# Kernel tuning notes

Measured on AMD Instinct MI355X. Metric: run time of the kernel, lower is better.

The kernel has to match this reference:

```python
import jax, jax.numpy as jnp
import numpy as np
from math import sqrt


def setup_inputs() -> dict:
    key = jax.random.key(0)
    kq, kk, kv = jax.random.split(key, 3)
    B, L, H, E = 4, 2048, 8, 64
    S, D = L, E
    return {
        "queries": jax.random.normal(kq, (B, L, H, E), dtype=jnp.float32),
        "keys": jax.random.normal(kk, (B, S, H, E), dtype=jnp.float32),
        "values": jax.random.normal(kv, (B, S, H, D), dtype=jnp.float32),
    }


def reference(queries, keys, values):
    # FullAttention with mask_flag=True (TriangularCausalMask), dropout p=0,
    # output_attention=False. scale = 1/sqrt(E).
    B, L, H, E = queries.shape
    S = keys.shape[1]
    scale = 1.0 / sqrt(E)
    # scores: [B, H, L, S]
    scores = jnp.einsum("blhe,bshe->bhls", queries, keys)
    # causal mask: positions s > l are masked (upper triangle above diagonal)
    causal = jnp.tril(jnp.ones((L, S), dtype=bool))  # True = keep
    neg_inf = jnp.finfo(scores.dtype).min
    scores = jnp.where(causal, scores, neg_inf)
    A = jax.nn.softmax(scale * scores, axis=-1)  # [B,H,L,S]
    # context: [B, L, H, D]
    V = jnp.einsum("bhls,bshd->blhd", A, values)
    return V
```

## Files before the change

kernel.cpp:

```cpp
#include <hip/hip_runtime.h>
#include <math.h>

#define BD 4
#define LD 2048
#define HD 8
#define ED 64
#define TQ 128
#define TK 64
#define RS (HD * ED)

typedef __attribute__((ext_vector_type(8))) _Float16 f16x8;
typedef __attribute__((ext_vector_type(4))) _Float16 f16x4;
typedef __attribute__((ext_vector_type(4))) float f32x4;
typedef __attribute__((ext_vector_type(4))) unsigned int u32x4;
typedef __attribute__((ext_vector_type(2))) unsigned int u32x2;
typedef unsigned int u32;
typedef unsigned long long u64;

__device__ inline u32 pkh(float a, float b) {
    return __builtin_bit_cast(u32, __builtin_amdgcn_cvt_pkrtz(a, b));
}
__device__ inline u64 pkh4(float a, float b, float c, float d) {
    return (u64)pkh(a, b) | ((u64)pkh(c, d) << 32);
}
__device__ inline int swz(int row, int bcol) {
    return row * 128 + ((((bcol >> 4) ^ row) & 7) << 4) + (bcol & 15);
}

__global__ __launch_bounds__(256, 2)
void fa_mfma_k16(const float* __restrict__ Q, const float* __restrict__ K,
                 const float* __restrict__ V, float* __restrict__ O) {
    __shared__ __align__(16) char smem[32768];

    const int t    = threadIdx.x;
    const int lane = t & 63;
    const int w    = t >> 6;
    const int m16  = lane & 15;
    const int quad = lane >> 4;

    const int b = blockIdx.x >> 3;
    const int h = blockIdx.x & 7;
    const int y   = (int)blockIdx.y;
    const int qtp = (y < 8) ? (15 - y) : (y - 8);
    const int q0  = qtp * TQ;
    const int kmax = 2 * qtp + 1;

    const int ks  = t >> 2;
    const int ke0 = (t & 3) << 2;
    const int vs0 = (t & 15) << 2;
    const int vd0 = (t >> 4) << 2;

    const float* Kbase = K + ((size_t)((b * LD + ks) * HD + h)) * ED + ke0;
    const float* Vbase = V + ((size_t)((b * LD + vs0) * HD + h)) * ED + vd0;

    const float qscale = 0.125f * 1.44269504088896340736f;
    f16x8 qf[2][2];
    #pragma unroll
    for (int sub = 0; sub < 2; ++sub) {
        const float* qrow =
            Q + ((size_t)((b * LD + q0 + (w << 5) + (sub << 4) + m16) * HD + h)) * ED;
        #pragma unroll
        for (int hf = 0; hf < 2; ++hf) {
            const float4 x = *(const float4*)(qrow + hf * 32 + quad * 8);
            const float4 y4 = *(const float4*)(qrow + hf * 32 + quad * 8 + 4);
            u32x4 p;
            p[0] = pkh(x.x * qscale, x.y * qscale);
            p[1] = pkh(x.z * qscale, x.w * qscale);
            p[2] = pkh(y4.x * qscale, y4.y * qscale);
            p[3] = pkh(y4.z * qscale, y4.w * qscale);
            qf[sub][hf] = __builtin_bit_cast(f16x8, p);
        }
    }

    f32x4 oacc[2][4];
    float l_i[2] = {0.0f, 0.0f};
    #pragma unroll
    for (int sub = 0; sub < 2; ++sub)
        #pragma unroll
        for (int nt = 0; nt < 4; ++nt) oacc[sub][nt] = (f32x4){0.f, 0.f, 0.f, 0.f};

    float4 kx[4], vx[4];
    {
        #pragma unroll
        for (int j = 0; j < 4; ++j) kx[j] = *(const float4*)(Kbase + 16 * j);
        #pragma unroll
        for (int r = 0; r < 4; ++r) vx[r] = *(const float4*)(Vbase + r * RS);
        char* wK = smem;
        char* wV = smem + 16384;
        #pragma unroll
        for (int j = 0; j < 4; ++j)
            *(u64*)(wK + swz(ks, 2 * (ke0 + 16 * j))) = pkh4(kx[j].x, kx[j].y, kx[j].z, kx[j].w);
        *(u64*)(wV + swz(vd0 + 0, 2 * vs0)) = pkh4(vx[0].x, vx[1].x, vx[2].x, vx[3].x);
        *(u64*)(wV + swz(vd0 + 1, 2 * vs0)) = pkh4(vx[0].y, vx[1].y, vx[2].y, vx[3].y);
        *(u64*)(wV + swz(vd0 + 2, 2 * vs0)) = pkh4(vx[0].z, vx[1].z, vx[2].z, vx[3].z);
        *(u64*)(wV + swz(vd0 + 3, 2 * vs0)) = pkh4(vx[0].w, vx[1].w, vx[2].w, vx[3].w);
    }
    __syncthreads();

    for (int kt = 0; kt <= kmax; ++kt) {
        char* rK = smem + ((kt & 1) << 13);
        char* rV = smem + 16384 + ((kt & 1) << 13);
        const bool pre = kt < kmax;

        if (pre) {
            const float* kp = Kbase + (size_t)(kt + 1) * (TK * RS);
            const float* vp = Vbase + (size_t)(kt + 1) * (TK * RS);
            #pragma unroll
            for (int j = 0; j < 4; ++j) kx[j] = *(const float4*)(kp + 16 * j);
            #pragma unroll
            for (int r = 0; r < 4; ++r) vx[r] = *(const float4*)(vp + r * RS);
        }

        const int offq = (2 * qtp - kt) * 64;
        if (offq + (w << 5) + 31 >= 0) {
            f32x4 sacc[2][4];
            #pragma unroll
            for (int kc = 0; kc < 4; ++kc) {
                const f16x8 kf0 = *(const f16x8*)(rK + swz(kc * 16 + m16, quad * 16));
                const f16x8 kf1 = *(const f16x8*)(rK + swz(kc * 16 + m16, 64 + quad * 16));
                #pragma unroll
                for (int sub = 0; sub < 2; ++sub) {
                    f32x4 z = {0.f, 0.f, 0.f, 0.f};
                    z = __builtin_amdgcn_mfma_f32_16x16x32_f16(kf0, qf[sub][0], z, 0, 0, 0);
                    z = __builtin_amdgcn_mfma_f32_16x16x32_f16(kf1, qf[sub][1], z, 0, 0, 0);
                    sacc[sub][kc] = z;
                }
            }

            if (offq < 64) {
                #pragma unroll
                for (int sub = 0; sub < 2; ++sub) {
                    const int ql = (w << 5) + (sub << 4) + m16 + offq;
                    #pragma unroll
                    for (int kc = 0; kc < 4; ++kc)
                        #pragma unroll
                        for (int i = 0; i < 4; ++i)
                            if (kc * 16 + quad * 4 + i > ql) sacc[sub][kc][i] = -INFINITY;
                }
            }

            f16x4 pf[2][4];
            #pragma unroll
            for (int sub = 0; sub < 2; ++sub) {
                #pragma unroll
                for (int kc = 0; kc < 4; ++kc) {
                    float p0 = __builtin_amdgcn_exp2f(sacc[sub][kc][0]);
                    float p1 = __builtin_amdgcn_exp2f(sacc[sub][kc][1]);
                    float p2 = __builtin_amdgcn_exp2f(sacc[sub][kc][2]);
                    float p3 = __builtin_amdgcn_exp2f(sacc[sub][kc][3]);
                    l_i[sub] += (p0 + p1) + (p2 + p3);
                    u32x2 pp;
                    pp[0] = pkh(p0, p1);
                    pp[1] = pkh(p2, p3);
                    pf[sub][kc] = __builtin_bit_cast(f16x4, pp);
                }
            }

            #pragma unroll
            for (int kc = 0; kc < 4; ++kc) {
                #pragma unroll
                for (int dt = 0; dt < 4; ++dt) {
                    const f16x4 vf = *(const f16x4*)
                        (rV + swz(dt * 16 + m16, 2 * (kc * 16 + quad * 4)));
                    oacc[0][dt] = __builtin_amdgcn_mfma_f32_16x16x16f16(vf, pf[0][kc], oacc[0][dt], 0, 0, 0);
                    oacc[1][dt] = __builtin_amdgcn_mfma_f32_16x16x16f16(vf, pf[1][kc], oacc[1][dt], 0, 0, 0);
                }
            }
        }

        if (pre) {
            char* wK = smem + ((kt & 1) ? 0 : 8192);
            char* wV = smem + 16384 + ((kt & 1) ? 0 : 8192);
            #pragma unroll
            for (int j = 0; j < 4; ++j)
                *(u64*)(wK + swz(ks, 2 * (ke0 + 16 * j))) = pkh4(kx[j].x, kx[j].y, kx[j].z, kx[j].w);
            *(u64*)(wV + swz(vd0 + 0, 2 * vs0)) = pkh4(vx[0].x, vx[1].x, vx[2].x, vx[3].x);
            *(u64*)(wV + swz(vd0 + 1, 2 * vs0)) = pkh4(vx[0].y, vx[1].y, vx[2].y, vx[3].y);
            *(u64*)(wV + swz(vd0 + 2, 2 * vs0)) = pkh4(vx[0].z, vx[1].z, vx[2].z, vx[3].z);
            *(u64*)(wV + swz(vd0 + 3, 2 * vs0)) = pkh4(vx[0].w, vx[1].w, vx[2].w, vx[3].w);
        }
        __syncthreads();
    }

    #pragma unroll
    for (int sub = 0; sub < 2; ++sub) {
        float l = l_i[sub];
        l += __shfl_xor(l, 16);
        l += __shfl_xor(l, 32);
        const float inv = 1.0f / l;
        float* orow =
            O + ((size_t)((b * LD + q0 + (w << 5) + (sub << 4) + m16) * HD + h)) * ED;
        #pragma unroll
        for (int dt = 0; dt < 4; ++dt) {
            float4 o;
            o.x = oacc[sub][dt][0] * inv;
            o.y = oacc[sub][dt][1] * inv;
            o.z = oacc[sub][dt][2] * inv;
            o.w = oacc[sub][dt][3] * inv;
            *(float4*)(orow + dt * 16 + quad * 4) = o;
        }
    }
}

extern "C" void kernel_launch(void* const* d_in, const int* in_sizes, int n_in,
                              void* d_out, int out_size, void* d_ws, size_t ws_size,
                              hipStream_t stream) {
    const float* Q = (const float*)d_in[0];
    const float* K = (const float*)d_in[1];
    const float* V = (const float*)d_in[2];
    float* O = (float*)d_out;
    dim3 grid(BD * HD, LD / TQ);
    fa_mfma_k16<<<grid, 256, 0, stream>>>(Q, K, V, O);
}
```

Baseline: 122.4 us.

## Split KV range across two blocks and combine bf16 partials in second kernel

Splits each query tile's causal key range into two halves processed by separate blocks (grid z=2). Each half writes unnormalized bf16 partial outputs and row sums to workspace, and a combine kernel sums them and normalizes. Occupancy hint is raised to 4 blocks per CU. The aim is to double the number of blocks and balance the causal workload. The cost is an extra kernel launch, the workspace traffic, and bf16 rounding of the partials. The split is safe without a max rescale only because the kernel already skips the running max and relies on the fixed scaled score range.

```diff
diff --git a/kernel.cpp b/kernel.cpp
--- a/kernel.cpp
+++ b/kernel.cpp
@@ -23,13 +23,23 @@
 __device__ inline u64 pkh4(float a, float b, float c, float d) {
     return (u64)pkh(a, b) | ((u64)pkh(c, d) << 32);
 }
+__device__ inline u32 f2bf(float f) {
+    u32 u = __builtin_bit_cast(u32, f);
+    u += 0x7fffu + ((u >> 16) & 1u);
+    return u >> 16;
+}
+__device__ inline float b2f(unsigned short s) {
+    return __builtin_bit_cast(float, (u32)s << 16);
+}
 __device__ inline int swz(int row, int bcol) {
     return row * 128 + ((((bcol >> 4) ^ row) & 7) << 4) + (bcol & 15);
 }
 
-__global__ __launch_bounds__(256, 2)
-void fa_mfma_k16(const float* __restrict__ Q, const float* __restrict__ K,
-                 const float* __restrict__ V, float* __restrict__ O) {
+template<int NSPLIT>
+__global__ __launch_bounds__(256, 4)
+void fa_fwd(const float* __restrict__ Q, const float* __restrict__ K,
+            const float* __restrict__ V, float* __restrict__ O,
+            unsigned short* __restrict__ Op, float* __restrict__ lp) {
     __shared__ __align__(16) char smem[32768];
 
     const int t    = threadIdx.x;
@@ -43,7 +53,10 @@
     const int y   = (int)blockIdx.y;
     const int qtp = (y < 8) ? (15 - y) : (y - 8);
     const int q0  = qtp * TQ;
-    const int kmax = 2 * qtp + 1;
+    const int split  = (int)blockIdx.z;
+    const int cnt    = (2 * qtp + 2) / NSPLIT;
+    const int kt0    = split * cnt;
+    const int kt_end = kt0 + cnt - 1;
 
     const int ks  = t >> 2;
     const int ke0 = (t & 3) << 2;
@@ -77,16 +90,18 @@
     #pragma unroll
     for (int sub = 0; sub < 2; ++sub)
         #pragma unroll
-        for (int nt = 0; nt < 4; ++nt) oacc[sub][nt] = (f32x4){0.f, 0.f, 0.f, 0.f};
+        for (int dt = 0; dt < 4; ++dt) oacc[sub][dt] = (f32x4){0.f, 0.f, 0.f, 0.f};
 
     float4 kx[4], vx[4];
     {
-        #pragma unroll
-        for (int j = 0; j < 4; ++j) kx[j] = *(const float4*)(Kbase + 16 * j);
-        #pragma unroll
-        for (int r = 0; r < 4; ++r) vx[r] = *(const float4*)(Vbase + r * RS);
-        char* wK = smem;
-        char* wV = smem + 16384;
+        const float* kp = Kbase + (size_t)kt0 * (TK * RS);
+        const float* vp = Vbase + (size_t)kt0 * (TK * RS);
+        #pragma unroll
+        for (int j = 0; j < 4; ++j) kx[j] = *(const float4*)(kp + 16 * j);
+        #pragma unroll
+        for (int r = 0; r < 4; ++r) vx[r] = *(const float4*)(vp + r * RS);
+        char* wK = smem + ((kt0 & 1) << 13);
+        char* wV = smem + 16384 + ((kt0 & 1) << 13);
         #pragma unroll
         for (int j = 0; j < 4; ++j)
             *(u64*)(wK + swz(ks, 2 * (ke0 + 16 * j))) = pkh4(kx[j].x, kx[j].y, kx[j].z, kx[j].w);
@@ -97,10 +112,10 @@
     }
     __syncthreads();
 
-    for (int kt = 0; kt <= kmax; ++kt) {
+    for (int kt = kt0; kt <= kt_end; ++kt) {
         char* rK = smem + ((kt & 1) << 13);
         char* rV = smem + 16384 + ((kt & 1) << 13);
-        const bool pre = kt < kmax;
+        const bool pre = kt < kt_end;
 
         if (pre) {
             const float* kp = Kbase + (size_t)(kt + 1) * (TK * RS);
@@ -144,10 +159,10 @@
             for (int sub = 0; sub < 2; ++sub) {
                 #pragma unroll
                 for (int kc = 0; kc < 4; ++kc) {
-                    float p0 = __builtin_amdgcn_exp2f(sacc[sub][kc][0]);
-                    float p1 = __builtin_amdgcn_exp2f(sacc[sub][kc][1]);
-                    float p2 = __builtin_amdgcn_exp2f(sacc[sub][kc][2]);
-                    float p3 = __builtin_amdgcn_exp2f(sacc[sub][kc][3]);
+                    const float p0 = __builtin_amdgcn_exp2f(sacc[sub][kc][0]);
+                    const float p1 = __builtin_amdgcn_exp2f(sacc[sub][kc][1]);
+                    const float p2 = __builtin_amdgcn_exp2f(sacc[sub][kc][2]);
+                    const float p3 = __builtin_amdgcn_exp2f(sacc[sub][kc][3]);
                     l_i[sub] += (p0 + p1) + (p2 + p3);
                     u32x2 pp;
                     pp[0] = pkh(p0, p1);
@@ -169,8 +184,8 @@
         }
 
         if (pre) {
-            char* wK = smem + ((kt & 1) ? 0 : 8192);
-            char* wV = smem + 16384 + ((kt & 1) ? 0 : 8192);
+            char* wK = smem + (((kt & 1) ^ 1) << 13);
+            char* wV = smem + 16384 + (((kt & 1) ^ 1) << 13);
             #pragma unroll
             for (int j = 0; j < 4; ++j)
                 *(u64*)(wK + swz(ks, 2 * (ke0 + 16 * j))) = pkh4(kx[j].x, kx[j].y, kx[j].z, kx[j].w);
@@ -187,19 +202,54 @@
         float l = l_i[sub];
         l += __shfl_xor(l, 16);
         l += __shfl_xor(l, 32);
-        const float inv = 1.0f / l;
-        float* orow =
-            O + ((size_t)((b * LD + q0 + (w << 5) + (sub << 4) + m16) * HD + h)) * ED;
-        #pragma unroll
-        for (int dt = 0; dt < 4; ++dt) {
-            float4 o;
-            o.x = oacc[sub][dt][0] * inv;
-            o.y = oacc[sub][dt][1] * inv;
-            o.z = oacc[sub][dt][2] * inv;
-            o.w = oacc[sub][dt][3] * inv;
-            *(float4*)(orow + dt * 16 + quad * 4) = o;
-        }
-    }
+        const int q = q0 + (w << 5) + (sub << 4) + m16;
+        if (NSPLIT == 1) {
+            const float inv = 1.0f / l;
+            float* orow = O + ((size_t)((b * LD + q) * HD + h)) * ED;
+            #pragma unroll
+            for (int dt = 0; dt < 4; ++dt) {
+                float4 o;
+                o.x = oacc[sub][dt][0] * inv;
+                o.y = oacc[sub][dt][1] * inv;
+                o.z = oacc[sub][dt][2] * inv;
+                o.w = oacc[sub][dt][3] * inv;
+                *(float4*)(orow + dt * 16 + quad * 4) = o;
+            }
+        } else {
+            unsigned short* prow = Op + (size_t)split * (BD * LD * HD * ED)
+                                      + ((size_t)((b * LD + q) * HD + h)) * ED;
+            #pragma unroll
+            for (int dt = 0; dt < 4; ++dt) {
+                const u64 pk = (u64)(f2bf(oacc[sub][dt][0]) | (f2bf(oacc[sub][dt][1]) << 16))
+                             | ((u64)(f2bf(oacc[sub][dt][2]) | (f2bf(oacc[sub][dt][3]) << 16)) << 32);
+                *(u64*)(prow + dt * 16 + quad * 4) = pk;
+            }
+            if (quad == 0)
+                lp[(size_t)split * (BD * HD * LD) + (b * HD + h) * LD + q] = l;
+        }
+    }
+}
+
+__global__ __launch_bounds__(256)
+void fa_combine(const unsigned short* __restrict__ Op,
+                const float* __restrict__ lp, float* __restrict__ O) {
+    const int tid = blockIdx.x * 256 + threadIdx.x;
+    const int rid = tid >> 4;
+    const int h   = rid & 7;
+    const int bq  = rid >> 3;
+    const int b   = bq >> 11;
+    const int q   = bq & 2047;
+    const int lidx = (b * HD + h) * LD + q;
+    const float inv = 1.0f / (lp[lidx] + lp[BD * HD * LD + lidx]);
+    const size_t i = (size_t)tid * 4;
+    const ushort4 a = *(const ushort4*)(Op + i);
+    const ushort4 c = *(const ushort4*)(Op + (size_t)(BD * LD * HD * ED) + i);
+    float4 o;
+    o.x = (b2f(a.x) + b2f(c.x)) * inv;
+    o.y = (b2f(a.y) + b2f(c.y)) * inv;
+    o.z = (b2f(a.z) + b2f(c.z)) * inv;
+    o.w = (b2f(a.w) + b2f(c.w)) * inv;
+    *(float4*)(O + i) = o;
 }
 
 extern "C" void kernel_launch(void* const* d_in, const int* in_sizes, int n_in,
@@ -209,6 +259,17 @@
     const float* K = (const float*)d_in[1];
     const float* V = (const float*)d_in[2];
     float* O = (float*)d_out;
-    dim3 grid(BD * HD, LD / TQ);
-    fa_mfma_k16<<<grid, 256, 0, stream>>>(Q, K, V, O);
-}
+    const size_t PSZ = (size_t)BD * LD * HD * ED;
+    const size_t need = 2 * PSZ * sizeof(unsigned short)
+                      + 2 * (size_t)BD * HD * LD * sizeof(float);
+    if (ws_size >= need) {
+        unsigned short* Op = (unsigned short*)d_ws;
+        float* lp = (float*)((char*)d_ws + 2 * PSZ * sizeof(unsigned short));
+        dim3 g1(BD * HD, 16, 2);
+        fa_fwd<2><<<g1, 256, 0, stream>>>(Q, K, V, nullptr, Op, lp);
+        fa_combine<<<(int)(PSZ / 4 / 256), 256, 0, stream>>>(Op, lp, O);
+    } else {
+        dim3 g1(BD * HD, 16, 1);
+        fa_fwd<1><<<g1, 256, 0, stream>>>(Q, K, V, O, nullptr, nullptr);
+    }
+}
```

After: 193.7 us. +58.3%, slower.

## Pre-convert K/V to swizzled fp16 tiles and stream them via direct-to-LDS loads

Applied to the files above, without the earlier changes.

Adds a prep kernel that converts K and V to fp16 once per tile, writing them into the swizzled (and, for V, transposed) shared-memory image in a workspace. The main kernel then fills shared memory with global_load_lds DMA copies instead of loading fp32, converting and storing through registers. It also halves the query tile to 64 rows with 128-thread blocks, which doubles the block count. This is meant to remove the repeated fp32 K/V reads and the per-block conversion cost. In exchange it adds a second launch and a workspace round trip, and it relies on the workspace being large enough.

```diff
diff --git a/kernel.cpp b/kernel.cpp
--- a/kernel.cpp
+++ b/kernel.cpp
@@ -5,9 +5,10 @@
 #define LD 2048
 #define HD 8
 #define ED 64
-#define TQ 128
+#define TQ 64
 #define TK 64
 #define RS (HD * ED)
+#define NTILE (BD * HD * 32)
 
 typedef __attribute__((ext_vector_type(8))) _Float16 f16x8;
 typedef __attribute__((ext_vector_type(4))) _Float16 f16x4;
@@ -20,16 +21,62 @@
 __device__ inline u32 pkh(float a, float b) {
     return __builtin_bit_cast(u32, __builtin_amdgcn_cvt_pkrtz(a, b));
 }
-__device__ inline u64 pkh4(float a, float b, float c, float d) {
-    return (u64)pkh(a, b) | ((u64)pkh(c, d) << 32);
-}
 __device__ inline int swz(int row, int bcol) {
     return row * 128 + ((((bcol >> 4) ^ row) & 7) << 4) + (bcol & 15);
 }
-
-__global__ __launch_bounds__(256, 2)
-void fa_mfma_k16(const float* __restrict__ Q, const float* __restrict__ K,
-                 const float* __restrict__ V, float* __restrict__ O) {
+__device__ inline void dma16(const void* g, void* l) {
+    __builtin_amdgcn_global_load_lds(
+        (const __attribute__((address_space(1))) u32*)g,
+        (__attribute__((address_space(3))) u32*)l, 16, 0, 0);
+}
+
+__global__ __launch_bounds__(256, 4)
+void fa_prep(const float* __restrict__ K, const float* __restrict__ V,
+             unsigned short* __restrict__ Kh, unsigned short* __restrict__ Vh) {
+    __shared__ __align__(16) char vimg[8192];
+    const int bid = blockIdx.x;
+    const int kt  = bid & 31;
+    const int bh  = bid >> 5;
+    const int b   = bh >> 3;
+    const int h   = bh & 7;
+    const int t   = threadIdx.x;
+    const int s   = t >> 2;
+    const int e0  = (t & 3) << 4;
+
+    const float* krow = K + ((size_t)((b * LD + kt * TK + s) * HD + h)) * ED + e0;
+    const float* vrow = V + ((size_t)((b * LD + kt * TK + s) * HD + h)) * ED + e0;
+
+    char* kimg = (char*)(Kh + (size_t)bid * 4096);
+    #pragma unroll
+    for (int j = 0; j < 2; ++j) {
+        const float4 x = *(const float4*)(krow + 8 * j);
+        const float4 y = *(const float4*)(krow + 8 * j + 4);
+        u32x4 p;
+        p[0] = pkh(x.x, x.y); p[1] = pkh(x.z, x.w);
+        p[2] = pkh(y.x, y.y); p[3] = pkh(y.z, y.w);
+        *(u32x4*)(kimg + swz(s, 2 * e0 + 16 * j)) = p;
+    }
+
+    float va[16];
+    #pragma unroll
+    for (int j = 0; j < 4; ++j) {
+        const float4 x = *(const float4*)(vrow + 4 * j);
+        va[4 * j + 0] = x.x; va[4 * j + 1] = x.y;
+        va[4 * j + 2] = x.z; va[4 * j + 3] = x.w;
+    }
+    #pragma unroll
+    for (int c = 0; c < 16; ++c)
+        *(_Float16*)(vimg + swz(e0 + c, 2 * s)) = (_Float16)va[c];
+    __syncthreads();
+
+    char* vout = (char*)(Vh + (size_t)bid * 4096);
+    *(u32x4*)(vout + t * 32)      = *(const u32x4*)(vimg + t * 32);
+    *(u32x4*)(vout + t * 32 + 16) = *(const u32x4*)(vimg + t * 32 + 16);
+}
+
+__global__ __launch_bounds__(128, 2)
+void fa_main(const float* __restrict__ Q, const unsigned short* __restrict__ Kh,
+             const unsigned short* __restrict__ Vh, float* __restrict__ O) {
     __shared__ __align__(16) char smem[32768];
 
     const int t    = threadIdx.x;
@@ -40,18 +87,12 @@
 
     const int b = blockIdx.x >> 3;
     const int h = blockIdx.x & 7;
-    const int y   = (int)blockIdx.y;
-    const int qtp = (y < 8) ? (15 - y) : (y - 8);
-    const int q0  = qtp * TQ;
-    const int kmax = 2 * qtp + 1;
-
-    const int ks  = t >> 2;
-    const int ke0 = (t & 3) << 2;
-    const int vs0 = (t & 15) << 2;
-    const int vd0 = (t >> 4) << 2;
-
-    const float* Kbase = K + ((size_t)((b * LD + ks) * HD + h)) * ED + ke0;
-    const float* Vbase = V + ((size_t)((b * LD + vs0) * HD + h)) * ED + vd0;
+    const int y  = (int)blockIdx.y;
+    const int qt = (y < 16) ? (31 - y) : (y - 16);
+    const int q0 = qt * TQ;
+
+    const char* Kt = (const char*)(Kh + ((size_t)(b * 8 + h) * 32) * 4096);
+    const char* Vt = (const char*)(Vh + ((size_t)(b * 8 + h) * 32) * 4096);
 
     const float qscale = 0.125f * 1.44269504088896340736f;
     f16x8 qf[2][2];
@@ -77,108 +118,85 @@
     #pragma unroll
     for (int sub = 0; sub < 2; ++sub)
         #pragma unroll
-        for (int nt = 0; nt < 4; ++nt) oacc[sub][nt] = (f32x4){0.f, 0.f, 0.f, 0.f};
-
-    float4 kx[4], vx[4];
-    {
-        #pragma unroll
-        for (int j = 0; j < 4; ++j) kx[j] = *(const float4*)(Kbase + 16 * j);
-        #pragma unroll
-        for (int r = 0; r < 4; ++r) vx[r] = *(const float4*)(Vbase + r * RS);
-        char* wK = smem;
-        char* wV = smem + 16384;
-        #pragma unroll
-        for (int j = 0; j < 4; ++j)
-            *(u64*)(wK + swz(ks, 2 * (ke0 + 16 * j))) = pkh4(kx[j].x, kx[j].y, kx[j].z, kx[j].w);
-        *(u64*)(wV + swz(vd0 + 0, 2 * vs0)) = pkh4(vx[0].x, vx[1].x, vx[2].x, vx[3].x);
-        *(u64*)(wV + swz(vd0 + 1, 2 * vs0)) = pkh4(vx[0].y, vx[1].y, vx[2].y, vx[3].y);
-        *(u64*)(wV + swz(vd0 + 2, 2 * vs0)) = pkh4(vx[0].z, vx[1].z, vx[2].z, vx[3].z);
-        *(u64*)(wV + swz(vd0 + 3, 2 * vs0)) = pkh4(vx[0].w, vx[1].w, vx[2].w, vx[3].w);
-    }
+        for (int dt = 0; dt < 4; ++dt) oacc[sub][dt] = (f32x4){0.f, 0.f, 0.f, 0.f};
+
+    const int woff = (w << 12) + lane * 16;
+    #define STAGE(ktile, buf)                                              \
+        {                                                                  \
+            const char* kg = Kt + (size_t)(ktile) * 8192 + woff;           \
+            const char* vg = Vt + (size_t)(ktile) * 8192 + woff;           \
+            char* kl = smem + ((buf) << 13) + woff;                        \
+            char* vl = smem + 16384 + ((buf) << 13) + woff;                \
+            _Pragma("unroll")                                              \
+            for (int i = 0; i < 4; ++i) {                                  \
+                dma16(kg + i * 1024, kl + i * 1024);                       \
+                dma16(vg + i * 1024, vl + i * 1024);                       \
+            }                                                              \
+        }
+
+    STAGE(0, 0);
     __syncthreads();
 
-    for (int kt = 0; kt <= kmax; ++kt) {
-        char* rK = smem + ((kt & 1) << 13);
-        char* rV = smem + 16384 + ((kt & 1) << 13);
-        const bool pre = kt < kmax;
-
-        if (pre) {
-            const float* kp = Kbase + (size_t)(kt + 1) * (TK * RS);
-            const float* vp = Vbase + (size_t)(kt + 1) * (TK * RS);
-            #pragma unroll
-            for (int j = 0; j < 4; ++j) kx[j] = *(const float4*)(kp + 16 * j);
-            #pragma unroll
-            for (int r = 0; r < 4; ++r) vx[r] = *(const float4*)(vp + r * RS);
-        }
-
-        const int offq = (2 * qtp - kt) * 64;
-        if (offq + (w << 5) + 31 >= 0) {
-            f32x4 sacc[2][4];
+    for (int kt = 0; kt <= qt; ++kt) {
+        if (kt < qt) STAGE(kt + 1, (kt + 1) & 1);
+
+        const char* rK = smem + ((kt & 1) << 13);
+        const char* rV = smem + 16384 + ((kt & 1) << 13);
+
+        f32x4 sacc[2][4];
+        #pragma unroll
+        for (int kc = 0; kc < 4; ++kc) {
+            const f16x8 kf0 = *(const f16x8*)(rK + swz(kc * 16 + m16, quad * 16));
+            const f16x8 kf1 = *(const f16x8*)(rK + swz(kc * 16 + m16, 64 + quad * 16));
+            #pragma unroll
+            for (int sub = 0; sub < 2; ++sub) {
+                f32x4 z = {0.f, 0.f, 0.f, 0.f};
+                z = __builtin_amdgcn_mfma_f32_16x16x32_f16(kf0, qf[sub][0], z, 0, 0, 0);
+                z = __builtin_amdgcn_mfma_f32_16x16x32_f16(kf1, qf[sub][1], z, 0, 0, 0);
+                sacc[sub][kc] = z;
+            }
+        }
+
+        if (kt == qt) {
+            #pragma unroll
+            for (int sub = 0; sub < 2; ++sub) {
+                const int ql = (w << 5) + (sub << 4) + m16;
+                #pragma unroll
+                for (int kc = 0; kc < 4; ++kc)
+                    #pragma unroll
+                    for (int i = 0; i < 4; ++i)
+                        if (kc * 16 + quad * 4 + i > ql) sacc[sub][kc][i] = -INFINITY;
+            }
+        }
+
+        f16x4 pf[2][4];
+        #pragma unroll
+        for (int sub = 0; sub < 2; ++sub) {
             #pragma unroll
             for (int kc = 0; kc < 4; ++kc) {
-                const f16x8 kf0 = *(const f16x8*)(rK + swz(kc * 16 + m16, quad * 16));
-                const f16x8 kf1 = *(const f16x8*)(rK + swz(kc * 16 + m16, 64 + quad * 16));
-                #pragma unroll
-                for (int sub = 0; sub < 2; ++sub) {
-                    f32x4 z = {0.f, 0.f, 0.f, 0.f};
-                    z = __builtin_amdgcn_mfma_f32_16x16x32_f16(kf0, qf[sub][0], z, 0, 0, 0);
-                    z = __builtin_amdgcn_mfma_f32_16x16x32_f16(kf1, qf[sub][1], z, 0, 0, 0);
-                    sacc[sub][kc] = z;
-                }
-            }
-
-            if (offq < 64) {
-                #pragma unroll
-                for (int sub = 0; sub < 2; ++sub) {
-                    const int ql = (w << 5) + (sub << 4) + m16 + offq;
-                    #pragma unroll
-                    for (int kc = 0; kc < 4; ++kc)
-                        #pragma unroll
-                        for (int i = 0; i < 4; ++i)
-                            if (kc * 16 + quad * 4 + i > ql) sacc[sub][kc][i] = -INFINITY;
-                }
-            }
-
-            f16x4 pf[2][4];
-            #pragma unroll
-            for (int sub = 0; sub < 2; ++sub) {
-                #pragma unroll
-                for (int kc = 0; kc < 4; ++kc) {
-                    float p0 = __builtin_amdgcn_exp2f(sacc[sub][kc][0]);
-                    float p1 = __builtin_amdgcn_exp2f(sacc[sub][kc][1]);
-                    float p2 = __builtin_amdgcn_exp2f(sacc[sub][kc][2]);
-                    float p3 = __builtin_amdgcn_exp2f(sacc[sub][kc][3]);
-                    l_i[sub] += (p0 + p1) + (p2 + p3);
-                    u32x2 pp;
-                    pp[0] = pkh(p0, p1);
-                    pp[1] = pkh(p2, p3);
-                    pf[sub][kc] = __builtin_bit_cast(f16x4, pp);
-                }
-            }
-
-            #pragma unroll
-            for (int kc = 0; kc < 4; ++kc) {
-                #pragma unroll
-                for (int dt = 0; dt < 4; ++dt) {
-                    const f16x4 vf = *(const f16x4*)
-                        (rV + swz(dt * 16 + m16, 2 * (kc * 16 + quad * 4)));
-                    oacc[0][dt] = __builtin_amdgcn_mfma_f32_16x16x16f16(vf, pf[0][kc], oacc[0][dt], 0, 0, 0);
-                    oacc[1][dt] = __builtin_amdgcn_mfma_f32_16x16x16f16(vf, pf[1][kc], oacc[1][dt], 0, 0, 0);
-                }
-            }
-        }
-
-        if (pre) {
-            char* wK = smem + ((kt & 1) ? 0 : 8192);
-            char* wV = smem + 16384 + ((kt & 1) ? 0 : 8192);
-            #pragma unroll
-            for (int j = 0; j < 4; ++j)
-                *(u64*)(wK + swz(ks, 2 * (ke0 + 16 * j))) = pkh4(kx[j].x, kx[j].y, kx[j].z, kx[j].w);
-            *(u64*)(wV + swz(vd0 + 0, 2 * vs0)) = pkh4(vx[0].x, vx[1].x, vx[2].x, vx[3].x);
-            *(u64*)(wV + swz(vd0 + 1, 2 * vs0)) = pkh4(vx[0].y, vx[1].y, vx[2].y, vx[3].y);
-            *(u64*)(wV + swz(vd0 + 2, 2 * vs0)) = pkh4(vx[0].z, vx[1].z, vx[2].z, vx[3].z);
-            *(u64*)(wV + swz(vd0 + 3, 2 * vs0)) = pkh4(vx[0].w, vx[1].w, vx[2].w, vx[3].w);
-        }
+                const float p0 = __builtin_amdgcn_exp2f(sacc[sub][kc][0]);
+                const float p1 = __builtin_amdgcn_exp2f(sacc[sub][kc][1]);
+                const float p2 = __builtin_amdgcn_exp2f(sacc[sub][kc][2]);
+                const float p3 = __builtin_amdgcn_exp2f(sacc[sub][kc][3]);
+                l_i[sub] += (p0 + p1) + (p2 + p3);
+                u32x2 pp;
+                pp[0] = pkh(p0, p1);
+                pp[1] = pkh(p2, p3);
+                pf[sub][kc] = __builtin_bit_cast(f16x4, pp);
+            }
+        }
+
+        #pragma unroll
+        for (int kc = 0; kc < 4; ++kc) {
+            #pragma unroll
+            for (int dt = 0; dt < 4; ++dt) {
+                const f16x4 vf = *(const f16x4*)
+                    (rV + swz(dt * 16 + m16, 2 * (kc * 16 + quad * 4)));
+                oacc[0][dt] = __builtin_amdgcn_mfma_f32_16x16x16f16(vf, pf[0][kc], oacc[0][dt], 0, 0, 0);
+                oacc[1][dt] = __builtin_amdgcn_mfma_f32_16x16x16f16(vf, pf[1][kc], oacc[1][dt], 0, 0, 0);
+            }
+        }
+
         __syncthreads();
     }
 
@@ -209,6 +227,9 @@
     const float* K = (const float*)d_in[1];
     const float* V = (const float*)d_in[2];
     float* O = (float*)d_out;
-    dim3 grid(BD * HD, LD / TQ);
-    fa_mfma_k16<<<grid, 256, 0, stream>>>(Q, K, V, O);
-}
+    unsigned short* Kh = (unsigned short*)d_ws;
+    unsigned short* Vh = Kh + (size_t)NTILE * 4096;
+    fa_prep<<<NTILE, 256, 0, stream>>>(K, V, Kh, Vh);
+    dim3 g2(BD * HD, 32);
+    fa_main<<<g2, 128, 0, stream>>>(Q, Kh, Vh, O);
+}
```

Measured after the change: 126.6 us. 3.5% more time.
